# Performance work log

Measured on AMD Instinct MI355X. Metric: run time of the kernel, lower is better.

The kernel has to match this reference:

```python
import jax, jax.numpy as jnp
import numpy as np
import math

N_EMBD = 1024
N_HEAD = 16
B, T = 4, 2048

def setup_inputs() -> dict:
    key = jax.random.key(0)
    k1, k2, k3, k4, k5 = jax.random.split(key, 5)
    C = N_EMBD
    scale_in = 1.0 / math.sqrt(C)
    x = jax.random.normal(k1, (B, T, C), dtype=jnp.float32)
    W_attn = jax.random.normal(k2, (C, 3 * C), dtype=jnp.float32) * scale_in
    b_attn = jax.random.normal(k3, (3 * C,), dtype=jnp.float32) * 0.02
    W_proj = jax.random.normal(k4, (C, C), dtype=jnp.float32) * scale_in
    b_proj = jax.random.normal(k5, (C,), dtype=jnp.float32) * 0.02
    attention_mask = jnp.ones((B, T), dtype=jnp.int32)
    return {"x": x, "W_attn": W_attn, "b_attn": b_attn,
            "W_proj": W_proj, "b_proj": b_proj,
            "attention_mask": attention_mask}

def reference(x, W_attn, b_attn, W_proj, b_proj, attention_mask):
    Bx, Tx, C = x.shape
    H = N_HEAD
    D = C // H
    qkv = x @ W_attn + b_attn                      # [B,T,3C]
    q, k, v = jnp.split(qkv, 3, axis=-1)
    # [B,H,T,D]
    q = q.reshape(Bx, Tx, H, D).transpose(0, 2, 1, 3)
    k = k.reshape(Bx, Tx, H, D).transpose(0, 2, 1, 3)
    v = v.reshape(Bx, Tx, H, D).transpose(0, 2, 1, 3)
    att = jnp.einsum('bhqd,bhkd->bhqk', q, k) * (1.0 / math.sqrt(D))
    causal = jnp.tril(jnp.ones((Tx, Tx), dtype=bool))  # [T,T]
    neg_inf = jnp.float32(-jnp.inf)
    att = jnp.where(causal[None, None, :, :], att, neg_inf)
    pad = (attention_mask != 0)[:, None, None, :]      # [B,1,1,T]
    att = jnp.where(pad, att, neg_inf)
    att = jax.nn.softmax(att, axis=-1)
    y = jnp.einsum('bhqk,bhkd->bhqd', att, v)          # [B,H,T,D]
    y = y.transpose(0, 2, 1, 3).reshape(Bx, Tx, C)
    y = y @ W_proj + b_proj
    return y
```

## Files before the change

kernel.cpp:

```cpp
#include <hip/hip_runtime.h>
#include <hip/hip_bf16.h>
#include <stdint.h>

#define B_ 4
#define T_ 2048
#define C_ 1024
#define H_ 16
#define D_ 64
#define BH_ (B_*H_)
#define M_ (B_*T_)

typedef __attribute__((ext_vector_type(8))) short short8;
typedef __attribute__((ext_vector_type(4))) float f32x4;
typedef __attribute__((ext_vector_type(16))) float f32x16;

#if __has_builtin(__builtin_amdgcn_exp2f)
#define EXP2(x) __builtin_amdgcn_exp2f(x)
#else
#define EXP2(x) exp2f(x)
#endif

#define QSCALE 0.18033688011112043f

__device__ __forceinline__ unsigned short f2bf(float f) {
  union { float f; unsigned int u; } v; v.f = f;
  unsigned int r = v.u + 0x7FFFu + ((v.u >> 16) & 1u);
  return (unsigned short)(r >> 16);
}

__device__ __forceinline__ unsigned int cvtpk_bf16(float lo, float hi) {
  unsigned int r;
  asm("v_cvt_pk_bf16_f32 %0, %1, %2" : "=v"(r) : "v"(lo), "v"(hi));
  return r;
}

__device__ __forceinline__ void gload_lds16(const void* g, void* l) {
  __builtin_amdgcn_global_load_lds(
      (__attribute__((address_space(1))) void*)g,
      (__attribute__((address_space(3))) void*)l, 16, 0, 0);
}

__global__ __launch_bounds__(256) void k_cvt(const float* __restrict__ in,
                                             unsigned short* __restrict__ out, int n) {
  int i = (blockIdx.x * 256 + threadIdx.x) * 4;
  if (i >= n) return;
  float4 v = *reinterpret_cast<const float4*>(in + i);
  union { unsigned short u[4]; unsigned long long ll; } o;
  o.u[0] = f2bf(v.x); o.u[1] = f2bf(v.y); o.u[2] = f2bf(v.z); o.u[3] = f2bf(v.w);
  *reinterpret_cast<unsigned long long*>(out + i) = o.ll;
}

__global__ __launch_bounds__(256) void k_tr(const float* __restrict__ W,
                                            unsigned short* __restrict__ Wt, int K, int N) {
  __shared__ float t[32][33];
  int n0 = blockIdx.x * 32, k0 = blockIdx.y * 32;
  int tx = threadIdx.x, ty = threadIdx.y;
  #pragma unroll
  for (int j = 0; j < 4; j++)
    t[ty + j*8][tx] = W[(size_t)(k0 + ty + j*8) * N + n0 + tx];
  __syncthreads();
  #pragma unroll
  for (int j = 0; j < 4; j++)
    Wt[(size_t)(n0 + ty + j*8) * K + k0 + tx] = f2bf(t[tx][ty + j*8]);
}

template<int QKV>
__global__ __launch_bounds__(256) void k_gemm4(const unsigned short* __restrict__ A,
                                               const unsigned short* __restrict__ Bt,
                                               const float* __restrict__ bias,
                                               void* __restrict__ outp, int N, int K) {
  __shared__ __align__(16) unsigned short Al[2][128*64];
  __shared__ __align__(16) unsigned short Bl[2][128*64];

  const int tid = threadIdx.x;
  const int lane = tid & 63, wv = tid >> 6;
  const int lg = lane >> 4, lr = lane & 15;
  const int wm = wv >> 1, wn = wv & 1;

  const int nwg = gridDim.x * gridDim.y;
  const int l = blockIdx.y * gridDim.x + blockIdx.x;
  const int wg = (l & 7) * (nwg >> 3) + (l >> 3);
  const int m0 = (wg / gridDim.x) * 128;
  const int n0 = (wg % gridDim.x) * 128;

  const int NT = K >> 6;

  auto stageA = [&](int s, int t) {
    #pragma unroll
    for (int u = 0; u < 4; ++u) {
      int gi = tid + u*256;
      int row = gi >> 3, g = gi & 7;
      gload_lds16(A + (size_t)(m0 + row) * K + t*64 + (g ^ (row & 7)) * 8,
                  (char*)Al[s] + gi*16);
    }
  };
  auto stageB = [&](int s, int t) {
    #pragma unroll
    for (int u = 0; u < 4; ++u) {
      int gi = tid + u*256;
      int row = gi >> 3, g = gi & 7;
      gload_lds16(Bt + (size_t)(n0 + row) * K + t*64 + (g ^ (row & 7)) * 8,
                  (char*)Bl[s] + gi*16);
    }
  };

  f32x4 acc[4][4];
  #pragma unroll
  for (int i = 0; i < 4; ++i)
    #pragma unroll
    for (int j = 0; j < 4; ++j) acc[i][j] = (f32x4){0.f, 0.f, 0.f, 0.f};

  stageA(0, 0); stageB(0, 0);
  asm volatile("s_waitcnt vmcnt(0)" ::: "memory");
  __builtin_amdgcn_s_barrier();

  for (int t = 0; t < NT; ++t) {
    const char* Asb = (const char*)Al[t & 1];
    const char* Bsb = (const char*)Bl[t & 1];
    const int s1 = (t & 1) ^ 1;
    const bool sn = (t + 1 < NT);
    short8 af[2][2], ag[2][2], bf[4][2];

    #pragma unroll
    for (int mf = 0; mf < 2; ++mf) {
      int row = wm*64 + mf*16 + lr; int r7 = row & 7;
      af[mf][0] = *(const short8*)(Asb + row*128 + ((lg      ^ r7) << 4));
      af[mf][1] = *(const short8*)(Asb + row*128 + (((4|lg) ^ r7) << 4));
    }
    #pragma unroll
    for (int nf = 0; nf < 4; ++nf) {
      int col = wn*64 + nf*16 + lr; int c7 = col & 7;
      bf[nf][0] = *(const short8*)(Bsb + col*128 + ((lg      ^ c7) << 4));
      bf[nf][1] = *(const short8*)(Bsb + col*128 + (((4|lg) ^ c7) << 4));
    }
    if (sn) stageA(s1, t + 1);
    __builtin_amdgcn_s_barrier();
    asm volatile("s_waitcnt lgkmcnt(0)" ::: "memory");
    __builtin_amdgcn_sched_barrier(0);
    __builtin_amdgcn_s_setprio(1);
    #pragma unroll
    for (int kh = 0; kh < 2; ++kh)
      #pragma unroll
      for (int mf = 0; mf < 2; ++mf)
        #pragma unroll
        for (int nf = 0; nf < 4; ++nf)
          acc[mf][nf] = __builtin_amdgcn_mfma_f32_16x16x32_bf16(
              af[mf][kh], bf[nf][kh], acc[mf][nf], 0, 0, 0);
    __builtin_amdgcn_s_setprio(0);
    __builtin_amdgcn_s_barrier();

    #pragma unroll
    for (int mf = 0; mf < 2; ++mf) {
      int row = wm*64 + (mf+2)*16 + lr; int r7 = row & 7;
      ag[mf][0] = *(const short8*)(Asb + row*128 + ((lg      ^ r7) << 4));
      ag[mf][1] = *(const short8*)(Asb + row*128 + (((4|lg) ^ r7) << 4));
    }
    if (sn) stageB(s1, t + 1);
    __builtin_amdgcn_s_barrier();
    asm volatile("s_waitcnt lgkmcnt(0)" ::: "memory");
    __builtin_amdgcn_sched_barrier(0);
    __builtin_amdgcn_s_setprio(1);
    #pragma unroll
    for (int kh = 0; kh < 2; ++kh)
      #pragma unroll
      for (int mf = 0; mf < 2; ++mf)
        #pragma unroll
        for (int nf = 0; nf < 4; ++nf)
          acc[mf+2][nf] = __builtin_amdgcn_mfma_f32_16x16x32_bf16(
              ag[mf][kh], bf[nf][kh], acc[mf+2][nf], 0, 0, 0);
    __builtin_amdgcn_s_setprio(0);
    asm volatile("s_waitcnt vmcnt(0)" ::: "memory");
    __builtin_amdgcn_s_barrier();
  }

  if (QKV) {
    unsigned short* qb = (unsigned short*)outp;
    const size_t SZ = (size_t)BH_ * T_ * D_;
    #pragma unroll
    for (int i4 = 0; i4 < 4; ++i4) {
      int mb = m0 + wm*64 + i4*16 + lg*4;
      #pragma unroll
      for (int nf = 0; nf < 4; ++nf) {
        int n = n0 + wn*64 + nf*16 + lr;
        float bv = bias[n];
        int which = n >> 10, c = n & 1023, h = c >> 6, d = c & 63;
        unsigned short* base = qb + (size_t)which * SZ;
        #pragma unroll
        for (int r = 0; r < 4; ++r) {
          int m = mb + r;
          int bb2 = m >> 11, tt = m & 2047;
          float y = acc[i4][nf][r] + bv;
          if (which == 0) y *= QSCALE;
          base[((size_t)(bb2*H_ + h)*T_ + tt)*D_ + d] = f2bf(y);
        }
      }
    }
  } else {
    float* out = (float*)outp;
    #pragma unroll
    for (int i4 = 0; i4 < 4; ++i4) {
      int mb = m0 + wm*64 + i4*16 + lg*4;
      #pragma unroll
      for (int nf = 0; nf < 4; ++nf) {
        int n = n0 + wn*64 + nf*16 + lr;
        float bv = bias[n];
        #pragma unroll
        for (int r = 0; r < 4; ++r)
          out[(size_t)(mb + r)*N + n] = acc[i4][nf][r] + bv;
      }
    }
  }
}

__global__ __launch_bounds__(256, 2) void k_attn4(const unsigned short* __restrict__ Qb,
                                                  const unsigned short* __restrict__ Kb,
                                                  const unsigned short* __restrict__ Vb,
                                                  const int* __restrict__ amask,
                                                  unsigned short* __restrict__ Yb) {
  __shared__ __align__(16) char pool[65536];

  const int l = blockIdx.y * 16 + blockIdx.x;
  const int local = l >> 3;
  const int tq = 15 - (local >> 3);
  const int bh = (l & 7) * 8 + (local & 7);
  const int bb = bh >> 4, hh = bh & 15;

  const int tid = threadIdx.x;
  const int lane = tid & 63, w = tid >> 6;
  const int hi = lane >> 5, l31 = lane & 31;

  const unsigned short* Qh = Qb + (size_t)bh * (T_*D_);
  const unsigned short* Kh = Kb + (size_t)bh * (T_*D_);
  const unsigned short* Vh = Vb + (size_t)bh * (T_*D_);

  const int vp = tid & 63, vdb = tid >> 6;

  auto stage_load = [&](int i, int b, short8 (&sv)[4], int& nm0, int& nm1) {
    const int kv0 = i << 7;
    char* base = pool + b * 32768;
    #pragma unroll
    for (int s = 0; s < 4; ++s) {
      int gi = tid + s * 256;
      int row = gi >> 3, gc = gi & 7;
      gload_lds16(Kh + (size_t)(kv0 + row)*D_ + (gc ^ (row & 7)) * 8, base + gi * 16);
    }
    const unsigned short* vsrc = Vh + (size_t)(kv0 + 2*vp)*D_ + vdb*16;
    sv[0] = *reinterpret_cast<const short8*>(vsrc);
    sv[1] = *reinterpret_cast<const short8*>(vsrc + 8);
    sv[2] = *reinterpret_cast<const short8*>(vsrc + D_);
    sv[3] = *reinterpret_cast<const short8*>(vsrc + D_ + 8);
    nm0 = amask[bb*T_ + kv0 + lane];
    nm1 = amask[bb*T_ + kv0 + 64 + lane];
  };
  auto stage_write = [&](int b, const short8 (&sv)[4]) {
    unsigned int* vt = (unsigned int*)(pool + b * 32768 + 16384);
    #pragma unroll
    for (int j = 0; j < 16; ++j) {
      int d = vdb*16 + j;
      unsigned short lo = (unsigned short)((j < 8) ? sv[0][j] : sv[1][j-8]);
      unsigned short hv = (unsigned short)((j < 8) ? sv[2][j] : sv[3][j-8]);
      unsigned int wd = lo | ((unsigned int)hv << 16);
      int pcol = (((vp >> 2) ^ (d & 15)) << 2) | (vp & 3);
      vt[d * 64 + pcol] = wd;
    }
  };

  const int nT = tq + 1;
  const int qbase = tq << 7;
  const int qw = qbase + w * 32;
  const int q  = qw + l31;

  short8 qf[4];
  #pragma unroll
  for (int dt = 0; dt < 4; ++dt)
    qf[dt] = *reinterpret_cast<const short8*>(Qh + (size_t)q*D_ + dt*16 + hi*8);

  f32x16 o0, o1;
  #pragma unroll
  for (int r = 0; r < 16; ++r) { o0[r] = 0.f; o1[r] = 0.f; }
  float mr = 0.f, ls = 0.f;

  short8 sv[4]; int cm0, cm1;
  stage_load(0, 0, sv, cm0, cm1);
  stage_write(0, sv);
  __syncthreads();

  for (int i = 0; i < nT; ++i) {
    const int b = i & 1;
    const bool pf = (i + 1 < nT);
    short8 nv[4]; int nm0 = 0, nm1 = 0;
    if (pf) stage_load(i + 1, b ^ 1, nv, nm0, nm1);
    const int kv0 = i << 7;

    const unsigned short* Klb = (const unsigned short*)(pool + b * 32768);
    const char* Vtb = pool + b * 32768 + 16384;

    f32x16 st[4];
    #pragma unroll
    for (int tl = 0; tl < 4; ++tl)
      #pragma unroll
      for (int r = 0; r < 16; ++r) st[tl][r] = 0.f;
    __builtin_amdgcn_s_setprio(1);
    #pragma unroll
    for (int dt = 0; dt < 4; ++dt) {
      int gg = dt * 2 + hi;
      #pragma unroll
      for (int tl = 0; tl < 4; ++tl) {
        int ra = tl*32 + l31;
        short8 kf = *reinterpret_cast<const short8*>(Klb + ra*64 + ((gg ^ (ra & 7)) * 8));
        st[tl] = __builtin_amdgcn_mfma_f32_32x32x16_bf16(kf, qf[dt], st[tl], 0, 0, 0);
      }
    }
    __builtin_amdgcn_s_setprio(0);

    if (kv0 + 127 > qw) {
      #pragma unroll
      for (int tl = 0; tl < 4; ++tl)
        #pragma unroll
        for (int r = 0; r < 16; ++r) {
          int kvl = tl*32 + (r & 3) + 8 * (r >> 2) + 4 * hi;
          if (kv0 + kvl > q) st[tl][r] = -1e30f;
        }
    }
    unsigned long long mb0 = __ballot(cm0 != 0);
    unsigned long long mb1 = __ballot(cm1 != 0);
    if ((mb0 & mb1) != ~0ull) {
      #pragma unroll
      for (int tl = 0; tl < 4; ++tl) {
        unsigned long long mb = (tl < 2) ? mb0 : mb1;
        int sh0 = (tl & 1) * 32;
        #pragma unroll
        for (int r = 0; r < 16; ++r) {
          int kvl = (r & 3) + 8 * (r >> 2) + 4 * hi;
          if (!((mb >> (kvl + sh0)) & 1)) st[tl][r] = -1e30f;
        }
      }
    }

    float rp[8];
    #pragma unroll
    for (int r = 0; r < 8; ++r) rp[r] = 0.f;
    #pragma unroll
    for (int tl = 0; tl < 4; ++tl)
      #pragma unroll
      for (int r = 0; r < 16; ++r) {
        st[tl][r] = EXP2(st[tl][r] - mr);
        rp[r & 7] += st[tl][r];
      }
    float rs = ((rp[0] + rp[1]) + (rp[2] + rp[3])) + ((rp[4] + rp[5]) + (rp[6] + rp[7]));
    rs += __shfl_xor(rs, 32);

    unsigned int pw[4][4][2];
    #pragma unroll
    for (int tl = 0; tl < 4; ++tl)
      #pragma unroll
      for (int a = 0; a < 4; ++a) {
        pw[tl][a][0] = cvtpk_bf16(st[tl][4*a],   st[tl][4*a+1]);
        pw[tl][a][1] = cvtpk_bf16(st[tl][4*a+2], st[tl][4*a+3]);
      }

    #pragma unroll
    for (int kt = 0; kt < 8; ++kt) {
      const int t = kt >> 1, h2 = kt & 1;
      unsigned int send0 = hi ? pw[t][2*h2][0]   : pw[t][2*h2+1][0];
      unsigned int send1 = hi ? pw[t][2*h2][1]   : pw[t][2*h2+1][1];
      unsigned int own0  = hi ? pw[t][2*h2+1][0] : pw[t][2*h2][0];
      unsigned int own1  = hi ? pw[t][2*h2+1][1] : pw[t][2*h2][1];
      unsigned int recv0 = __shfl_xor(send0, 32);
      unsigned int recv1 = __shfl_xor(send1, 32);
      union { unsigned int u[4]; short8 v; } pf2;
      pf2.u[0] = hi ? recv0 : own0;
      pf2.u[1] = hi ? recv1 : own1;
      pf2.u[2] = hi ? own0  : recv0;
      pf2.u[3] = hi ? own1  : recv1;
      int gg = kt * 2 + hi;
      int dA = l31;
      short8 vf0 = *reinterpret_cast<const short8*>(Vtb + dA*256 + ((gg ^ (dA & 15)) * 16));
      int dB = 32 + l31;
      short8 vf1 = *reinterpret_cast<const short8*>(Vtb + dB*256 + ((gg ^ (dB & 15)) * 16));
      __builtin_amdgcn_s_setprio(1);
      o0 = __builtin_amdgcn_mfma_f32_32x32x16_bf16(vf0, pf2.v, o0, 0, 0, 0);
      o1 = __builtin_amdgcn_mfma_f32_32x32x16_bf16(vf1, pf2.v, o1, 0, 0, 0);
      __builtin_amdgcn_s_setprio(0);
    }

    if (__all(rs <= 65536.f)) {
      ls += rs;
    } else {
      float lgf;
      asm("v_log_f32 %0, %1" : "=v"(lgf) : "v"(rs));
      int lgi = (int)lgf + 1;
      float corr = __int_as_float((unsigned)(127 - lgi) << 23);
      mr += (float)lgi;
      ls = (ls + rs) * corr;
      #pragma unroll
      for (int r = 0; r < 16; ++r) { o0[r] *= corr; o1[r] *= corr; }
    }

    if (pf) { stage_write(b ^ 1, nv); cm0 = nm0; cm1 = nm1; }
    __syncthreads();
  }

  float inv = 1.0f / ls;
  size_t rowbase = ((size_t)bb*T_ + q)*C_ + hh*D_;
  #pragma unroll
  for (int a = 0; a < 4; ++a) {
    union { unsigned short h[4]; unsigned long long ll; } y0, y1;
    #pragma unroll
    for (int bq = 0; bq < 4; ++bq) {
      int r = 4*a + bq;
      y0.h[bq] = f2bf(o0[r] * inv);
      y1.h[bq] = f2bf(o1[r] * inv);
    }
    int d0o = 8*a + 4*hi;
    *reinterpret_cast<unsigned long long*>(Yb + rowbase + d0o)      = y0.ll;
    *reinterpret_cast<unsigned long long*>(Yb + rowbase + 32 + d0o) = y1.ll;
  }
}

extern "C" void kernel_launch(void* const* d_in, const int* in_sizes, int n_in,
                              void* d_out, int out_size, void* d_ws, size_t ws_size,
                              hipStream_t stream) {
  const float* x      = (const float*)d_in[0];
  const float* W_attn = (const float*)d_in[1];
  const float* b_attn = (const float*)d_in[2];
  const float* W_proj = (const float*)d_in[3];
  const float* b_proj = (const float*)d_in[4];
  const int*   amask  = (const int*)d_in[5];
  float* out = (float*)d_out;

  char* ws = (char*)d_ws;
  size_t off = 0;
  auto alloc = [&](size_t bytes) { char* p = ws + off; off += (bytes + 255) & ~(size_t)255; return p; };
  unsigned short* xb   = (unsigned short*)alloc((size_t)M_ * C_ * 2);
  unsigned short* Wta  = (unsigned short*)alloc((size_t)3 * C_ * C_ * 2);
  unsigned short* Wtp  = (unsigned short*)alloc((size_t)C_ * C_ * 2);
  unsigned short* qkvb = (unsigned short*)alloc((size_t)3 * BH_ * T_ * D_ * 2);
  unsigned short* Yb   = (unsigned short*)alloc((size_t)M_ * C_ * 2);

  k_cvt<<<(M_ * C_) / 1024, 256, 0, stream>>>(x, xb, M_ * C_);
  k_tr<<<dim3(3*C_/32, C_/32), dim3(32, 8), 0, stream>>>(W_attn, Wta, C_, 3*C_);
  k_tr<<<dim3(C_/32,  C_/32),  dim3(32, 8), 0, stream>>>(W_proj, Wtp, C_, C_);

  k_gemm4<1><<<dim3(3*C_/128, M_/128), 256, 0, stream>>>(xb, Wta, b_attn, qkvb, 3*C_, C_);

  unsigned short* Qb = qkvb;
  unsigned short* Kb = qkvb + (size_t)BH_ * T_ * D_;
  unsigned short* Vb = qkvb + 2 * (size_t)BH_ * T_ * D_;
  k_attn4<<<dim3(16, BH_), 256, 0, stream>>>(Qb, Kb, Vb, amask, Yb);

  k_gemm4<0><<<dim3(C_/128, M_/128), 256, 0, stream>>>(Yb, Wtp, b_proj, out, C_, C_);
}
```

Measured before the change: 162.5 us.

## Single-buffer V tile and split score tile to fit three blocks per CU

```diff
diff --git a/kernel.cpp b/kernel.cpp
--- a/kernel.cpp
+++ b/kernel.cpp
@@ -212,12 +212,12 @@
   }
 }
 
-__global__ __launch_bounds__(256, 2) void k_attn4(const unsigned short* __restrict__ Qb,
+__global__ __launch_bounds__(256, 3) void k_attn4(const unsigned short* __restrict__ Qb,
                                                   const unsigned short* __restrict__ Kb,
                                                   const unsigned short* __restrict__ Vb,
                                                   const int* __restrict__ amask,
                                                   unsigned short* __restrict__ Yb) {
-  __shared__ __align__(16) char pool[65536];
+  __shared__ __align__(16) char pool[49152];
 
   const int l = blockIdx.y * 16 + blockIdx.x;
   const int local = l >> 3;
@@ -235,9 +235,9 @@
 
   const int vp = tid & 63, vdb = tid >> 6;
 
-  auto stage_load = [&](int i, int b, short8 (&sv)[4], int& nm0, int& nm1) {
+  auto stage_load = [&](int i, int kb, short8 (&sv)[4], int& nm0, int& nm1) {
     const int kv0 = i << 7;
-    char* base = pool + b * 32768;
+    char* base = pool + kb * 16384;
     #pragma unroll
     for (int s = 0; s < 4; ++s) {
       int gi = tid + s * 256;
@@ -252,8 +252,8 @@
     nm0 = amask[bb*T_ + kv0 + lane];
     nm1 = amask[bb*T_ + kv0 + 64 + lane];
   };
-  auto stage_write = [&](int b, const short8 (&sv)[4]) {
-    unsigned int* vt = (unsigned int*)(pool + b * 32768 + 16384);
+  auto stage_write = [&](const short8 (&sv)[4]) {
+    unsigned int* vt = (unsigned int*)(pool + 32768);
     #pragma unroll
     for (int j = 0; j < 16; ++j) {
       int d = vdb*16 + j;
@@ -282,108 +282,111 @@
 
   short8 sv[4]; int cm0, cm1;
   stage_load(0, 0, sv, cm0, cm1);
-  stage_write(0, sv);
+  stage_write(sv);
   __syncthreads();
 
+  int kb = 0;
   for (int i = 0; i < nT; ++i) {
-    const int b = i & 1;
     const bool pf = (i + 1 < nT);
     short8 nv[4]; int nm0 = 0, nm1 = 0;
-    if (pf) stage_load(i + 1, b ^ 1, nv, nm0, nm1);
+    if (pf) stage_load(i + 1, kb ^ 1, nv, nm0, nm1);
     const int kv0 = i << 7;
 
-    const unsigned short* Klb = (const unsigned short*)(pool + b * 32768);
-    const char* Vtb = pool + b * 32768 + 16384;
-
-    f32x16 st[4];
-    #pragma unroll
-    for (int tl = 0; tl < 4; ++tl)
-      #pragma unroll
-      for (int r = 0; r < 16; ++r) st[tl][r] = 0.f;
-    __builtin_amdgcn_s_setprio(1);
-    #pragma unroll
-    for (int dt = 0; dt < 4; ++dt) {
-      int gg = dt * 2 + hi;
-      #pragma unroll
-      for (int tl = 0; tl < 4; ++tl) {
-        int ra = tl*32 + l31;
-        short8 kf = *reinterpret_cast<const short8*>(Klb + ra*64 + ((gg ^ (ra & 7)) * 8));
-        st[tl] = __builtin_amdgcn_mfma_f32_32x32x16_bf16(kf, qf[dt], st[tl], 0, 0, 0);
-      }
-    }
-    __builtin_amdgcn_s_setprio(0);
-
-    if (kv0 + 127 > qw) {
-      #pragma unroll
-      for (int tl = 0; tl < 4; ++tl)
+    const unsigned short* Klb = (const unsigned short*)(pool + kb * 16384);
+    const char* Vtb = pool + 32768;
+    const bool diag = (kv0 + 127 > qw);
+    unsigned long long mbh[2];
+    mbh[0] = __ballot(cm0 != 0);
+    mbh[1] = __ballot(cm1 != 0);
+    float rs = 0.f;
+
+    #pragma unroll
+    for (int h = 0; h < 2; ++h) {
+      f32x16 st[2];
+      #pragma unroll
+      for (int u = 0; u < 2; ++u)
+        #pragma unroll
+        for (int r = 0; r < 16; ++r) st[u][r] = 0.f;
+      __builtin_amdgcn_s_setprio(1);
+      #pragma unroll
+      for (int dt = 0; dt < 4; ++dt) {
+        int gg = dt * 2 + hi;
+        #pragma unroll
+        for (int u = 0; u < 2; ++u) {
+          int ra = (2*h + u)*32 + l31;
+          short8 kf = *reinterpret_cast<const short8*>(Klb + ra*64 + ((gg ^ (ra & 7)) * 8));
+          st[u] = __builtin_amdgcn_mfma_f32_32x32x16_bf16(kf, qf[dt], st[u], 0, 0, 0);
+        }
+      }
+      __builtin_amdgcn_s_setprio(0);
+
+      if (diag) {
+        #pragma unroll
+        for (int u = 0; u < 2; ++u)
+          #pragma unroll
+          for (int r = 0; r < 16; ++r) {
+            int kvl = (2*h + u)*32 + (r & 3) + 8 * (r >> 2) + 4 * hi;
+            if (kv0 + kvl > q) st[u][r] = -1e30f;
+          }
+      }
+      if (mbh[h] != ~0ull) {
+        #pragma unroll
+        for (int u = 0; u < 2; ++u) {
+          int sh0 = u * 32;
+          #pragma unroll
+          for (int r = 0; r < 16; ++r) {
+            int kvl = (r & 3) + 8 * (r >> 2) + 4 * hi;
+            if (!((mbh[h] >> (kvl + sh0)) & 1)) st[u][r] = -1e30f;
+          }
+        }
+      }
+
+      float rp[4] = {0.f, 0.f, 0.f, 0.f};
+      #pragma unroll
+      for (int u = 0; u < 2; ++u)
         #pragma unroll
         for (int r = 0; r < 16; ++r) {
-          int kvl = tl*32 + (r & 3) + 8 * (r >> 2) + 4 * hi;
-          if (kv0 + kvl > q) st[tl][r] = -1e30f;
+          st[u][r] = EXP2(st[u][r] - mr);
+          rp[r & 3] += st[u][r];
         }
-    }
-    unsigned long long mb0 = __ballot(cm0 != 0);
-    unsigned long long mb1 = __ballot(cm1 != 0);
-    if ((mb0 & mb1) != ~0ull) {
-      #pragma unroll
-      for (int tl = 0; tl < 4; ++tl) {
-        unsigned long long mb = (tl < 2) ? mb0 : mb1;
-        int sh0 = (tl & 1) * 32;
-        #pragma unroll
-        for (int r = 0; r < 16; ++r) {
-          int kvl = (r & 3) + 8 * (r >> 2) + 4 * hi;
-          if (!((mb >> (kvl + sh0)) & 1)) st[tl][r] = -1e30f;
+      rs += (rp[0] + rp[1]) + (rp[2] + rp[3]);
+
+      unsigned int pw[2][4][2];
+      #pragma unroll
+      for (int u = 0; u < 2; ++u)
+        #pragma unroll
+        for (int a = 0; a < 4; ++a) {
+          pw[u][a][0] = cvtpk_bf16(st[u][4*a],   st[u][4*a+1]);
+          pw[u][a][1] = cvtpk_bf16(st[u][4*a+2], st[u][4*a+3]);
         }
-      }
-    }
-
-    float rp[8];
-    #pragma unroll
-    for (int r = 0; r < 8; ++r) rp[r] = 0.f;
-    #pragma unroll
-    for (int tl = 0; tl < 4; ++tl)
-      #pragma unroll
-      for (int r = 0; r < 16; ++r) {
-        st[tl][r] = EXP2(st[tl][r] - mr);
-        rp[r & 7] += st[tl][r];
-      }
-    float rs = ((rp[0] + rp[1]) + (rp[2] + rp[3])) + ((rp[4] + rp[5]) + (rp[6] + rp[7]));
+
+      #pragma unroll
+      for (int kl = 0; kl < 4; ++kl) {
+        const int u = kl >> 1, h2 = kl & 1;
+        unsigned int send0 = hi ? pw[u][2*h2][0]   : pw[u][2*h2+1][0];
+        unsigned int send1 = hi ? pw[u][2*h2][1]   : pw[u][2*h2+1][1];
+        unsigned int own0  = hi ? pw[u][2*h2+1][0] : pw[u][2*h2][0];
+        unsigned int own1  = hi ? pw[u][2*h2+1][1] : pw[u][2*h2][1];
+        unsigned int recv0 = __shfl_xor(send0, 32);
+        unsigned int recv1 = __shfl_xor(send1, 32);
+        union { unsigned int u4[4]; short8 v; } pf2;
+        pf2.u4[0] = hi ? recv0 : own0;
+        pf2.u4[1] = hi ? recv1 : own1;
+        pf2.u4[2] = hi ? own0  : recv0;
+        pf2.u4[3] = hi ? own1  : recv1;
+        int gg = ((2*h + u)*2 + h2)*2 + hi;
+        int dA = l31;
+        short8 vf0 = *reinterpret_cast<const short8*>(Vtb + dA*256 + ((gg ^ (dA & 15)) * 16));
+        int dB = 32 + l31;
+        short8 vf1 = *reinterpret_cast<const short8*>(Vtb + dB*256 + ((gg ^ (dB & 15)) * 16));
+        __builtin_amdgcn_s_setprio(1);
+        o0 = __builtin_amdgcn_mfma_f32_32x32x16_bf16(vf0, pf2.v, o0, 0, 0, 0);
+        o1 = __builtin_amdgcn_mfma_f32_32x32x16_bf16(vf1, pf2.v, o1, 0, 0, 0);
+        __builtin_amdgcn_s_setprio(0);
+      }
+    }
+
     rs += __shfl_xor(rs, 32);
-
-    unsigned int pw[4][4][2];
-    #pragma unroll
-    for (int tl = 0; tl < 4; ++tl)
-      #pragma unroll
-      for (int a = 0; a < 4; ++a) {
-        pw[tl][a][0] = cvtpk_bf16(st[tl][4*a],   st[tl][4*a+1]);
-        pw[tl][a][1] = cvtpk_bf16(st[tl][4*a+2], st[tl][4*a+3]);
-      }
-
-    #pragma unroll
-    for (int kt = 0; kt < 8; ++kt) {
-      const int t = kt >> 1, h2 = kt & 1;
-      unsigned int send0 = hi ? pw[t][2*h2][0]   : pw[t][2*h2+1][0];
-      unsigned int send1 = hi ? pw[t][2*h2][1]   : pw[t][2*h2+1][1];
-      unsigned int own0  = hi ? pw[t][2*h2+1][0] : pw[t][2*h2][0];
-      unsigned int own1  = hi ? pw[t][2*h2+1][1] : pw[t][2*h2][1];
-      unsigned int recv0 = __shfl_xor(send0, 32);
-      unsigned int recv1 = __shfl_xor(send1, 32);
-      union { unsigned int u[4]; short8 v; } pf2;
-      pf2.u[0] = hi ? recv0 : own0;
-      pf2.u[1] = hi ? recv1 : own1;
-      pf2.u[2] = hi ? own0  : recv0;
-      pf2.u[3] = hi ? own1  : recv1;
-      int gg = kt * 2 + hi;
-      int dA = l31;
-      short8 vf0 = *reinterpret_cast<const short8*>(Vtb + dA*256 + ((gg ^ (dA & 15)) * 16));
-      int dB = 32 + l31;
-      short8 vf1 = *reinterpret_cast<const short8*>(Vtb + dB*256 + ((gg ^ (dB & 15)) * 16));
-      __builtin_amdgcn_s_setprio(1);
-      o0 = __builtin_amdgcn_mfma_f32_32x32x16_bf16(vf0, pf2.v, o0, 0, 0, 0);
-      o1 = __builtin_amdgcn_mfma_f32_32x32x16_bf16(vf1, pf2.v, o1, 0, 0, 0);
-      __builtin_amdgcn_s_setprio(0);
-    }
-
     if (__all(rs <= 65536.f)) {
       ls += rs;
     } else {
@@ -397,8 +400,11 @@
       for (int r = 0; r < 16; ++r) { o0[r] *= corr; o1[r] *= corr; }
     }
 
-    if (pf) { stage_write(b ^ 1, nv); cm0 = nm0; cm1 = nm1; }
+    asm volatile("s_waitcnt lgkmcnt(0)" ::: "memory");
+    __builtin_amdgcn_s_barrier();
+    if (pf) { stage_write(nv); cm0 = nm0; cm1 = nm1; }
     __syncthreads();
+    kb ^= 1;
   }
 
   float inv = 1.0f / ls;
```

New measurement: 305.5 us. 1.88x slower.

## Store V transposed in QKV epilogue and async-load it directly into LDS

Applied to the files above, without the earlier changes.

```diff
diff --git a/kernel.cpp b/kernel.cpp
--- a/kernel.cpp
+++ b/kernel.cpp
@@ -133,7 +133,7 @@
       bf[nf][0] = *(const short8*)(Bsb + col*128 + ((lg      ^ c7) << 4));
       bf[nf][1] = *(const short8*)(Bsb + col*128 + (((4|lg) ^ c7) << 4));
     }
-    if (sn) stageA(s1, t + 1);
+    if (sn) { stageA(s1, t + 1); stageB(s1, t + 1); }
     __builtin_amdgcn_s_barrier();
     asm volatile("s_waitcnt lgkmcnt(0)" ::: "memory");
     __builtin_amdgcn_sched_barrier(0);
@@ -155,7 +155,6 @@
       ag[mf][0] = *(const short8*)(Asb + row*128 + ((lg      ^ r7) << 4));
       ag[mf][1] = *(const short8*)(Asb + row*128 + (((4|lg) ^ r7) << 4));
     }
-    if (sn) stageB(s1, t + 1);
     __builtin_amdgcn_s_barrier();
     asm volatile("s_waitcnt lgkmcnt(0)" ::: "memory");
     __builtin_amdgcn_sched_barrier(0);
@@ -184,14 +183,24 @@
         int n = n0 + wn*64 + nf*16 + lr;
         float bv = bias[n];
         int which = n >> 10, c = n & 1023, h = c >> 6, d = c & 63;
-        unsigned short* base = qb + (size_t)which * SZ;
-        #pragma unroll
-        for (int r = 0; r < 4; ++r) {
-          int m = mb + r;
-          int bb2 = m >> 11, tt = m & 2047;
-          float y = acc[i4][nf][r] + bv;
-          if (which == 0) y *= QSCALE;
-          base[((size_t)(bb2*H_ + h)*T_ + tt)*D_ + d] = f2bf(y);
+        if (which == 2) {
+          int bb2 = mb >> 11, tt = mb & 2047;
+          union { unsigned short h4[4]; unsigned long long ll; } pk;
+          #pragma unroll
+          for (int r = 0; r < 4; ++r) pk.h4[r] = f2bf(acc[i4][nf][r] + bv);
+          unsigned short* vbase = qb + 2 * SZ;
+          *reinterpret_cast<unsigned long long*>(
+              &vbase[((size_t)(bb2*H_ + h)*D_ + d)*T_ + tt]) = pk.ll;
+        } else {
+          unsigned short* base = qb + (size_t)which * SZ;
+          #pragma unroll
+          for (int r = 0; r < 4; ++r) {
+            int m = mb + r;
+            int bb2 = m >> 11, tt = m & 2047;
+            float y = acc[i4][nf][r] + bv;
+            if (which == 0) y *= QSCALE;
+            base[((size_t)(bb2*H_ + h)*T_ + tt)*D_ + d] = f2bf(y);
+          }
         }
       }
     }
@@ -233,9 +242,7 @@
   const unsigned short* Kh = Kb + (size_t)bh * (T_*D_);
   const unsigned short* Vh = Vb + (size_t)bh * (T_*D_);
 
-  const int vp = tid & 63, vdb = tid >> 6;
-
-  auto stage_load = [&](int i, int b, short8 (&sv)[4], int& nm0, int& nm1) {
+  auto stage_load = [&](int i, int b, int& nm0, int& nm1) {
     const int kv0 = i << 7;
     char* base = pool + b * 32768;
     #pragma unroll
@@ -244,25 +251,15 @@
       int row = gi >> 3, gc = gi & 7;
       gload_lds16(Kh + (size_t)(kv0 + row)*D_ + (gc ^ (row & 7)) * 8, base + gi * 16);
     }
-    const unsigned short* vsrc = Vh + (size_t)(kv0 + 2*vp)*D_ + vdb*16;
-    sv[0] = *reinterpret_cast<const short8*>(vsrc);
-    sv[1] = *reinterpret_cast<const short8*>(vsrc + 8);
-    sv[2] = *reinterpret_cast<const short8*>(vsrc + D_);
-    sv[3] = *reinterpret_cast<const short8*>(vsrc + D_ + 8);
+    #pragma unroll
+    for (int s = 0; s < 4; ++s) {
+      int gi = tid + s * 256;
+      int d = gi >> 4, q = gi & 15;
+      gload_lds16(Vh + (size_t)d*T_ + kv0 + ((q ^ (d & 15)) * 8),
+                  base + 16384 + gi * 16);
+    }
     nm0 = amask[bb*T_ + kv0 + lane];
     nm1 = amask[bb*T_ + kv0 + 64 + lane];
-  };
-  auto stage_write = [&](int b, const short8 (&sv)[4]) {
-    unsigned int* vt = (unsigned int*)(pool + b * 32768 + 16384);
-    #pragma unroll
-    for (int j = 0; j < 16; ++j) {
-      int d = vdb*16 + j;
-      unsigned short lo = (unsigned short)((j < 8) ? sv[0][j] : sv[1][j-8]);
-      unsigned short hv = (unsigned short)((j < 8) ? sv[2][j] : sv[3][j-8]);
-      unsigned int wd = lo | ((unsigned int)hv << 16);
-      int pcol = (((vp >> 2) ^ (d & 15)) << 2) | (vp & 3);
-      vt[d * 64 + pcol] = wd;
-    }
   };
 
   const int nT = tq + 1;
@@ -280,16 +277,15 @@
   for (int r = 0; r < 16; ++r) { o0[r] = 0.f; o1[r] = 0.f; }
   float mr = 0.f, ls = 0.f;
 
-  short8 sv[4]; int cm0, cm1;
-  stage_load(0, 0, sv, cm0, cm1);
-  stage_write(0, sv);
+  int cm0, cm1;
+  stage_load(0, 0, cm0, cm1);
   __syncthreads();
 
   for (int i = 0; i < nT; ++i) {
     const int b = i & 1;
     const bool pf = (i + 1 < nT);
-    short8 nv[4]; int nm0 = 0, nm1 = 0;
-    if (pf) stage_load(i + 1, b ^ 1, nv, nm0, nm1);
+    int nm0 = 0, nm1 = 0;
+    if (pf) stage_load(i + 1, b ^ 1, nm0, nm1);
     const int kv0 = i << 7;
 
     const unsigned short* Klb = (const unsigned short*)(pool + b * 32768);
@@ -397,7 +393,7 @@
       for (int r = 0; r < 16; ++r) { o0[r] *= corr; o1[r] *= corr; }
     }
 
-    if (pf) { stage_write(b ^ 1, nv); cm0 = nm0; cm1 = nm1; }
+    if (pf) { cm0 = nm0; cm1 = nm1; }
     __syncthreads();
   }
 
```

Result: no change. 162.1 us (median of 2 runs) (-0.2%).
